# Kernel tuning notes

Measured on AMD Instinct MI355X. Metric: run time of the kernel, lower is better.

The kernel has to match this reference:

```python
import jax, jax.numpy as jnp
import numpy as np

GAMMA = 0.9
SCALE_BASE = 512.0


def _xpos(x, downscale=False):
    """XPOS rotary embedding (torchscale variant) applied to x: (B, L, D)."""
    B, L, D = x.shape
    half = D // 2
    # per-channel magnitude base: ((2i) + 0.4*D) / (1.4*D), i over even channels
    scale_vec = (jnp.arange(0, D, 2, dtype=jnp.float32) + 0.4 * D) / (1.4 * D)  # (half,)
    power = jnp.arange(L, dtype=jnp.float32) / SCALE_BASE                        # (L,)
    scale = scale_vec[None, :] ** power[:, None]                                 # (L, half)
    if downscale:
        scale = 1.0 / scale
    # fixed sinusoidal frequencies over `half` dims
    inv_freq = 1.0 / (10000.0 ** (jnp.arange(half, dtype=jnp.float32) / half))   # (half,)
    sinusoid = jnp.arange(L, dtype=jnp.float32)[:, None] * inv_freq[None, :]     # (L, half)
    sin = jnp.repeat(jnp.sin(sinusoid) * scale, 2, axis=-1)                      # (L, D) interleaved dup
    cos = jnp.repeat(jnp.cos(sinusoid) * scale, 2, axis=-1)
    # rotate_every_two: (x0,x1,x2,x3,...) -> (-x1,x0,-x3,x2,...)
    x_even = x[..., 0::2]
    x_odd = x[..., 1::2]
    rot = jnp.stack((-x_odd, x_even), axis=-1).reshape(x.shape)
    return x * cos + rot * sin


def _get_D(seq_len):
    n = jnp.arange(seq_len, dtype=jnp.float32)[:, None]
    m = jnp.arange(seq_len, dtype=jnp.float32)[None, :]
    D = GAMMA ** jnp.abs(n - m)  # non-causal decay, no NaNs since gamma > 0
    return D


def setup_inputs() -> dict:
    key = jax.random.key(0)
    k1, k2, k3, k4 = jax.random.split(key, 4)
    B, L, H, Dh = 8, 2048, 1024, 1024
    X = jax.random.normal(k1, (B, L, H), dtype=jnp.float32)
    W_Q = jax.random.normal(k2, (H, Dh), dtype=jnp.float32) / H
    W_K = jax.random.normal(k3, (H, Dh), dtype=jnp.float32) / H
    W_V = jax.random.normal(k4, (H, Dh), dtype=jnp.float32) / H
    return {"X": X, "W_Q": W_Q, "W_K": W_K, "W_V": W_V}


def reference(X, W_Q, W_K, W_V):
    B, L, H = X.shape
    D = _get_D(L)                       # (L, L)
    Q = _xpos(X @ W_Q)                  # (B, L, Dh)
    K = _xpos(X @ W_K, downscale=True)  # (B, L, Dh)
    V = X @ W_V                         # (B, L, Dv)
    scores = jnp.einsum('bqd,bkd->bqk', Q, K)   # (B, L, L)
    p_attn = jax.nn.softmax(scores, axis=-1)
    p_attn = p_attn * D[None, :, :]              # elementwise decay AFTER softmax
    return jnp.einsum('bqk,bkv->bqv', p_attn, V)
```

## Files before the change

### kernel.cpp

```cpp
#include <hip/hip_runtime.h>
#include <math.h>


#define LDIM 2048
#define HDIM 1024
#define MTOT 16384

typedef unsigned short u16;
typedef unsigned int u32;
typedef __attribute__((ext_vector_type(16))) float f32x16;
typedef __attribute__((ext_vector_type(8))) short s16x8;

#define GLD16(gp, lp) __builtin_amdgcn_global_load_lds( \
    (const __attribute__((address_space(1))) void*)(gp), \
    (__attribute__((address_space(3))) void*)(lp), 16, 0, 0)

__device__ __forceinline__ u16 f2bf(float f) {
    unsigned u = __float_as_uint(f);
    return (u16)((u + 0x7FFFu + ((u >> 16) & 1u)) >> 16);
}

__device__ __forceinline__ void sincos_rev(float ang, float* sn, float* cs) {
    double dr = (double)ang * 0.15915494309189535;
    dr -= __builtin_floor(dr);
    float fr = (float)dr;
    float s_, c_;
    asm("v_sin_f32 %0, %1" : "=v"(s_) : "v"(fr));
    asm("v_cos_f32 %0, %1" : "=v"(c_) : "v"(fr));
    *sn = s_; *cs = c_;
}

#define ROW32(reg, laneHi) (((reg) & 3) + 8 * ((reg) >> 2) + 4 * (laneHi))

__device__ __forceinline__ void gemm256(const u16* __restrict__ A,
                                        const u16* __restrict__ B,
                                        int lda, int ldb, int K, int m0, int n0,
                                        char* smem, int tid, f32x16 (*acc)[2])
{
    const int wv = tid >> 6, ln = tid & 63;
    const int wm = wv >> 2, wn = wv & 3;
    const int lane31 = ln & 31, laneHi = ln >> 5;
    const int srow = tid >> 3;
    const int scol = ((tid & 7) ^ (srow & 7)) * 8;

    const u16* ap[4];
    const u16* bp[4];
#pragma unroll
    for (int r = 0; r < 4; ++r) {
        ap[r] = A + (size_t)(m0 + r * 64 + srow) * lda + scol;
        bp[r] = B + (size_t)(n0 + r * 64 + srow) * ldb + scol;
    }

    int abyte[4], bbyte[2];
    const int slot_r = (laneHi ^ (lane31 & 7)) << 4;
#pragma unroll
    for (int fm = 0; fm < 4; ++fm)
        abyte[fm] = (wm * 128 + fm * 32 + lane31) * 128 + slot_r;
#pragma unroll
    for (int fn = 0; fn < 2; ++fn)
        bbyte[fn] = 32768 + (wn * 64 + fn * 32 + lane31) * 128 + slot_r;

#define SGA0(e_) do{ char* d_=smem+(e_)*65536+tid*16;       GLD16(ap[0],d_); GLD16(ap[1],d_+8192); ap[0]+=64; ap[1]+=64; }while(0)
#define SGA1(e_) do{ char* d_=smem+(e_)*65536+16384+tid*16; GLD16(ap[2],d_); GLD16(ap[3],d_+8192); ap[2]+=64; ap[3]+=64; }while(0)
#define SGB0(e_) do{ char* d_=smem+(e_)*65536+32768+tid*16; GLD16(bp[0],d_); GLD16(bp[1],d_+8192); bp[0]+=64; bp[1]+=64; }while(0)
#define SGB1(e_) do{ char* d_=smem+(e_)*65536+49152+tid*16; GLD16(bp[2],d_); GLD16(bp[3],d_+8192); bp[2]+=64; bp[3]+=64; }while(0)

#define READS(Bb_, ks) do {                                                   \
        _Pragma("unroll") for (int fm_ = 0; fm_ < 4; ++fm_)                   \
            af[fm_] = *(const s16x8*)((Bb_) + (abyte[fm_] ^ ((ks) << 5)));    \
        _Pragma("unroll") for (int fn_ = 0; fn_ < 2; ++fn_)                   \
            bf[fn_] = *(const s16x8*)((Bb_) + (bbyte[fn_] ^ ((ks) << 5)));    \
    } while (0)

#define MFMA8 do { __builtin_amdgcn_s_setprio(1);                             \
        _Pragma("unroll") for (int fm_ = 0; fm_ < 4; ++fm_)                   \
            _Pragma("unroll") for (int fn_ = 0; fn_ < 2; ++fn_)               \
                acc[fm_][fn_] = __builtin_amdgcn_mfma_f32_32x32x16_bf16(      \
                    af[fm_], bf[fn_], acc[fm_][fn_], 0, 0, 0);                \
        __builtin_amdgcn_s_setprio(0); } while (0)

#define BAR do { __builtin_amdgcn_s_barrier();                                \
                 __builtin_amdgcn_sched_barrier(0); } while (0)

    const int nk = K >> 6;

    SGA0(0); SGB0(0); SGA1(0); SGB1(0);

#pragma unroll 1
    for (int t = 0; t < nk; ++t) {
        const int d = t & 1, e = d ^ 1;
        const bool pre = (t + 1 < nk);
        const char* Bb = smem + d * 65536;
        s16x8 af[4], bf[2];

        if (pre) { SGA0(e); asm volatile("s_waitcnt vmcnt(2)" ::: "memory"); }
        else     {          asm volatile("s_waitcnt vmcnt(0)" ::: "memory"); }
        BAR;
        READS(Bb, 0); if (pre) SGB0(e); BAR; MFMA8; BAR;
        READS(Bb, 1); if (pre) SGA1(e); BAR; MFMA8; BAR;
        READS(Bb, 2); if (pre) SGB1(e); BAR; MFMA8; BAR;
        READS(Bb, 3);                   BAR; MFMA8; BAR;
    }
    __syncthreads();
#undef SGA0
#undef SGA1
#undef SGB0
#undef SGB1
#undef READS
#undef MFMA8
#undef BAR
}

__global__ __launch_bounds__(256) void prep_all(
    const float* __restrict__ X,
    const float* __restrict__ Wq, const float* __restrict__ Wk,
    const float* __restrict__ Wv,
    u16* __restrict__ Xb, u16* __restrict__ WT,
    u32* __restrict__ CSq, u32* __restrict__ CSk)
{
    __shared__ float L[64][65];
    const int bid = blockIdx.x;
    if (bid < 2048) {
        const int n4 = MTOT * HDIM / 4;
        int i = bid * 256 + threadIdx.x;
        const int stride = 2048 * 256;
        for (; i < n4; i += stride) {
            float4 v = ((const float4*)X)[i];
            ushort4 o = make_ushort4(f2bf(v.x), f2bf(v.y), f2bf(v.z), f2bf(v.w));
            ((ushort4*)Xb)[i] = o;
        }
    } else if (bid < 4096) {
        const int l = bid - 2048;
        for (int ih = threadIdx.x; ih < 512; ih += 256) {
            float invf = exp2f(-13.287712379549449f * (1.f / 512.f) * (float)ih);
            float sn, cs;
            sincos_rev((float)l * invf, &sn, &cs);
            float l2sv = log2f(((float)(2 * ih) + 409.6f) * (1.f / 1433.6f));
            float e = (float)l * (1.f / 512.f) * l2sv;
            float sq = exp2f(e), sk = exp2f(-e);
            CSq[l * 512 + ih] = (u32)f2bf(cs * sq) | ((u32)f2bf(sn * sq) << 16);
            CSk[l * 512 + ih] = (u32)f2bf(cs * sk) | ((u32)f2bf(sn * sk) << 16);
        }
    } else {
        const int r = bid - 4096;
        const int z = r >> 8;
        const int y = (r >> 4) & 15;
        const int x = r & 15;
        const float* Wz = (z == 0) ? Wq : (z == 1) ? Wk : Wv;
        u16* Oz = WT + (size_t)z * HDIM * HDIM;
        const int k0 = y * 64, n0 = x * 64;
        const int t = threadIdx.x;
        const int r_ = t >> 4, c4 = (t & 15) * 4;
#pragma unroll
        for (int it = 0; it < 4; ++it) {
            const int row = it * 16 + r_;
            float4 v = *(const float4*)&Wz[(size_t)(k0 + row) * HDIM + n0 + c4];
            L[row][c4 + 0] = v.x; L[row][c4 + 1] = v.y;
            L[row][c4 + 2] = v.z; L[row][c4 + 3] = v.w;
        }
        __syncthreads();
#pragma unroll
        for (int it = 0; it < 4; ++it) {
            const int orow = it * 16 + r_;
            ushort4 o = make_ushort4(f2bf(L[c4 + 0][orow]), f2bf(L[c4 + 1][orow]),
                                     f2bf(L[c4 + 2][orow]), f2bf(L[c4 + 3][orow]));
            *(ushort4*)&Oz[(size_t)(n0 + orow) * HDIM + k0 + c4] = o;
        }
    }
}

__global__ __launch_bounds__(512, 2) void qkv_gemm(
    const u16* __restrict__ Xb, const u16* __restrict__ WT,
    const u32* __restrict__ CSq, const u32* __restrict__ CSk,
    u16* __restrict__ Qb, u16* __restrict__ Kb, u16* __restrict__ Vt)
{
    __shared__ __align__(16) char smem[256 * 264 * 2];
    const int bid = blockIdx.x;
    const int xcd = bid & 7, t = bid >> 3;
    const int m8 = t & 7;
    const int n_ = (t >> 3) & 3;
    const int z  = t >> 5;
    const int m0 = (xcd * 8 + m8) * 256;
    const int n0 = n_ * 256;
    const int tid = threadIdx.x;

    f32x16 acc[4][2] = {};

    gemm256(Xb, WT + (size_t)z * HDIM * HDIM, HDIM, HDIM, HDIM, m0, n0, smem, tid, acc);

    const int wv = tid >> 6, ln = tid & 63;
    const int wm = wv >> 2, wn = wv & 3;
    const int lane31 = ln & 31, laneHi = ln >> 5;
    const int l0 = m0 & (LDIM - 1);
    u16* T = (u16*)smem;

    if (z < 2) {
        const u32* CS = (z == 0) ? CSq : CSk;
#pragma unroll
        for (int fn = 0; fn < 2; ++fn) {
            const int gc = n0 + wn * 64 + fn * 32 + lane31;
            const int ih = gc >> 1;
            const float sgn = (gc & 1) ? 1.f : -1.f;
            const u32* tb = CS + (size_t)l0 * 512 + ih;
#pragma unroll
            for (int fm = 0; fm < 4; ++fm) {
#pragma unroll
                for (int reg = 0; reg < 16; ++reg) {
                    const int rowl = wm * 128 + fm * 32 + ROW32(reg, laneHi);
                    u32 v = tb[(size_t)rowl * 512];
                    float cs = __uint_as_float(v << 16);
                    float sn = __uint_as_float(v & 0xFFFF0000u);
                    float c = acc[fm][fn][reg];
                    float p = __shfl_xor(c, 1);
                    T[rowl * 264 + wn * 64 + fn * 32 + lane31] =
                        f2bf(c * cs + sgn * p * sn);
                }
            }
        }
        __syncthreads();
        u16* Out = (z == 0) ? Qb : Kb;
        const int row_ = tid >> 5, slot = tid & 31;
#pragma unroll
        for (int g = 0; g < 16; ++g) {
            const int row = g * 16 + row_;
            s16x8 v = *(const s16x8*)&T[row * 264 + slot * 8];
            *(s16x8*)&Out[(size_t)(m0 + row) * HDIM + n0 + slot * 8] = v;
        }
    } else {
#pragma unroll
        for (int fn = 0; fn < 2; ++fn)
#pragma unroll
            for (int fm = 0; fm < 4; ++fm)
#pragma unroll
                for (int reg = 0; reg < 16; ++reg)
                    T[(wn * 64 + fn * 32 + lane31) * 264 +
                      wm * 128 + fm * 32 + ROW32(reg, laneHi)] =
                        f2bf(acc[fm][fn][reg]);
        __syncthreads();
        const int b = m0 >> 11;
        const int row_ = tid >> 5, slot = tid & 31;
#pragma unroll
        for (int g = 0; g < 16; ++g) {
            const int row = g * 16 + row_;
            s16x8 v = *(const s16x8*)&T[row * 264 + slot * 8];
            *(s16x8*)&Vt[((size_t)b * HDIM + n0 + row) * LDIM + l0 + slot * 8] = v;
        }
    }
}

__global__ __launch_bounds__(512, 2) void qk_gemm(
    const u16* __restrict__ Q, const u16* __restrict__ Km,
    u16* __restrict__ Wm, float* __restrict__ Zp)
{
    __shared__ __align__(16) char smem[256 * 264 * 2];
    __shared__ float Zl[4][256];
    const int bid = blockIdx.x;
    const int b = bid & 7, t = bid >> 3;
    const int mt = t & 7;
    const int nt = t >> 3;
    const int m0 = mt * 256;
    const int n0 = nt * 256;
    const int tid = threadIdx.x;

    f32x16 acc[4][2] = {};

    gemm256(Q + (size_t)b * LDIM * HDIM, Km + (size_t)b * LDIM * HDIM,
            HDIM, HDIM, HDIM, m0, n0, smem, tid, acc);

    const int wv = tid >> 6, ln = tid & 63;
    const int wm = wv >> 2, wn = wv & 3;
    const int lane31 = ln & 31, laneHi = ln >> 5;
    u16* T = (u16*)smem;
    const float LOG2E = 1.4426950408889634f;
    const float LOG2G = -0.15200309344504997f;

#pragma unroll
    for (int fm = 0; fm < 4; ++fm) {
        float ps[16];
#pragma unroll
        for (int reg = 0; reg < 16; ++reg) ps[reg] = 0.f;
#pragma unroll
        for (int fn = 0; fn < 2; ++fn) {
            const int gk = n0 + wn * 64 + fn * 32 + lane31;
#pragma unroll
            for (int reg = 0; reg < 16; ++reg) {
                const int mloc = wm * 128 + fm * 32 + ROW32(reg, laneHi);
                const int gq = m0 + mloc;
                float t1 = acc[fm][fn][reg] * LOG2E;
                float e = exp2f(t1);
                int dd = gq - gk; dd = dd < 0 ? -dd : dd;
                ps[reg] += e;
                T[mloc * 264 + wn * 64 + fn * 32 + lane31] =
                    f2bf(exp2f(t1 + (float)dd * LOG2G));
            }
        }
#pragma unroll
        for (int reg = 0; reg < 16; ++reg) {
            float s = ps[reg];
            s += __shfl_xor(s, 1); s += __shfl_xor(s, 2);
            s += __shfl_xor(s, 4); s += __shfl_xor(s, 8);
            s += __shfl_xor(s, 16);
            if (lane31 == 0)
                Zl[wn][wm * 128 + fm * 32 + ROW32(reg, laneHi)] = s;
        }
    }
    __syncthreads();

    const int row_ = tid >> 5, slot = tid & 31;
#pragma unroll
    for (int g = 0; g < 16; ++g) {
        const int row = g * 16 + row_;
        s16x8 v = *(const s16x8*)&T[row * 264 + slot * 8];
        *(s16x8*)&Wm[((size_t)b * LDIM + m0 + row) * LDIM + n0 + slot * 8] = v;
    }
    if (tid < 256)
        Zp[((size_t)b * 8 + nt) * LDIM + m0 + tid] =
            Zl[0][tid] + Zl[1][tid] + Zl[2][tid] + Zl[3][tid];
}

__global__ __launch_bounds__(512, 2) void pv_gemm(
    const u16* __restrict__ Wm, const u16* __restrict__ Vt,
    const float* __restrict__ Zp, float* __restrict__ Out)
{
    __shared__ __align__(16) char smem[2 * 65536];
    __shared__ float Zinv[256];
    const int bid = blockIdx.x;
    const int b = bid & 7, t = bid >> 3;
    const int mt4 = t & 3;
    const int nt = (t >> 2) & 3;
    const int mtH = t >> 4;
    const int m0 = (mtH * 4 + mt4) * 256;
    const int n0 = nt * 256;
    const int tid = threadIdx.x;

    if (tid < 256) {
        float zz = 0.f;
#pragma unroll
        for (int nb = 0; nb < 8; ++nb)
            zz += Zp[((size_t)b * 8 + nb) * LDIM + m0 + tid];
        Zinv[tid] = 1.0f / zz;
    }
    __syncthreads();

    f32x16 acc[4][2] = {};

    gemm256(Wm + (size_t)b * LDIM * LDIM, Vt + (size_t)b * HDIM * LDIM,
            LDIM, LDIM, LDIM, m0, n0, smem, tid, acc);

    const int wv = tid >> 6, ln = tid & 63;
    const int wm = wv >> 2, wn = wv & 3;
    const int lane31 = ln & 31, laneHi = ln >> 5;
    float* Ob = Out + (size_t)b * LDIM * HDIM;
#pragma unroll
    for (int fm = 0; fm < 4; ++fm)
#pragma unroll
        for (int fn = 0; fn < 2; ++fn) {
            const int gn = n0 + wn * 64 + fn * 32 + lane31;
#pragma unroll
            for (int reg = 0; reg < 16; ++reg) {
                const int row = wm * 128 + fm * 32 + ROW32(reg, laneHi);
                Ob[(size_t)(m0 + row) * HDIM + gn] = acc[fm][fn][reg] * Zinv[row];
            }
        }
}

extern "C" void kernel_launch(void* const* d_in, const int* in_sizes, int n_in,
                              void* d_out, int out_size, void* d_ws, size_t ws_size,
                              hipStream_t stream)
{
    (void)in_sizes; (void)n_in; (void)out_size; (void)ws_size;
    const float* X  = (const float*)d_in[0];
    const float* Wq = (const float*)d_in[1];
    const float* Wk = (const float*)d_in[2];
    const float* Wv = (const float*)d_in[3];
    char* ws = (char*)d_ws;
    const size_t MB = 1024 * 1024;

    u16* Wmat = (u16*)ws;
    u16* Xb   = (u16*)ws;
    u16* WT   = (u16*)(ws + 32 * MB);
    u16* Qb   = (u16*)(ws + 64 * MB);
    u16* Kb   = (u16*)(ws + 96 * MB);
    u16* Vt   = (u16*)(ws + 128 * MB);
    float* Zp = (float*)(ws + 160 * MB);
    u32* CSq  = (u32*)(ws + 161 * MB);
    u32* CSk  = (u32*)(ws + 165 * MB);

    prep_all<<<4864, 256, 0, stream>>>(X, Wq, Wk, Wv, Xb, WT, CSq, CSk);
    qkv_gemm<<<768, 512, 0, stream>>>(Xb, WT, CSq, CSk, Qb, Kb, Vt);
    qk_gemm<<<512, 512, 0, stream>>>(Qb, Kb, Wmat, Zp);
    pv_gemm<<<256, 512, 0, stream>>>(Wmat, Vt, Zp, (float*)d_out);
}
```

Baseline: 334.3 us.

## Switch GEMMs to 16x16x32 MFMA with quadrant-ordered register reuse

Replaces the 32x32x16 bf16 MFMA tiles with 16x16x32 tiles in all three GEMMs and rewrites the LDS read and MFMA schedule into quadrant order, so A and B fragments are reused across sub-tiles. The prefetch of the next stage's B half is issued earlier. All epilogues are remapped to the new accumulator layout, and the V transpose store is vectorized. The aim is higher MFMA throughput and fewer LDS reads per MFMA, at the cost of more live fragment registers.

```diff
diff --git a/kernel.cpp b/kernel.cpp
--- a/kernel.cpp
+++ b/kernel.cpp
@@ -8,7 +8,7 @@
 
 typedef unsigned short u16;
 typedef unsigned int u32;
-typedef __attribute__((ext_vector_type(16))) float f32x16;
+typedef __attribute__((ext_vector_type(4))) float f32x4;
 typedef __attribute__((ext_vector_type(8))) short s16x8;
 
 #define GLD16(gp, lp) __builtin_amdgcn_global_load_lds( \
@@ -30,16 +30,14 @@
     *sn = s_; *cs = c_;
 }
 
-#define ROW32(reg, laneHi) (((reg) & 3) + 8 * ((reg) >> 2) + 4 * (laneHi))
-
-__device__ __forceinline__ void gemm256(const u16* __restrict__ A,
-                                        const u16* __restrict__ B,
-                                        int lda, int ldb, int K, int m0, int n0,
-                                        char* smem, int tid, f32x16 (*acc)[2])
+__device__ __forceinline__ void gemm256q(const u16* __restrict__ A,
+                                         const u16* __restrict__ B,
+                                         int lda, int ldb, int K, int m0, int n0,
+                                         char* smem, int tid, f32x4 (*acc)[4])
 {
     const int wv = tid >> 6, ln = tid & 63;
     const int wm = wv >> 2, wn = wv & 3;
-    const int lane31 = ln & 31, laneHi = ln >> 5;
+    const int lr = ln & 15, lg = ln >> 4;
     const int srow = tid >> 3;
     const int scol = ((tid & 7) ^ (srow & 7)) * 8;
 
@@ -51,63 +49,79 @@
         bp[r] = B + (size_t)(n0 + r * 64 + srow) * ldb + scol;
     }
 
-    int abyte[4], bbyte[2];
-    const int slot_r = (laneHi ^ (lane31 & 7)) << 4;
-#pragma unroll
-    for (int fm = 0; fm < 4; ++fm)
-        abyte[fm] = (wm * 128 + fm * 32 + lane31) * 128 + slot_r;
-#pragma unroll
-    for (int fn = 0; fn < 2; ++fn)
-        bbyte[fn] = 32768 + (wn * 64 + fn * 32 + lane31) * 128 + slot_r;
+    int arow[8], brow[4];
+#pragma unroll
+    for (int fm = 0; fm < 8; ++fm) arow[fm] = (wm * 128 + fm * 16 + lr) * 128;
+#pragma unroll
+    for (int fn = 0; fn < 4; ++fn) brow[fn] = 32768 + (wn * 64 + fn * 16 + lr) * 128;
+    int slotb[2];
+#pragma unroll
+    for (int kk = 0; kk < 2; ++kk) slotb[kk] = (((kk << 2) | lg) ^ (lr & 7)) << 4;
 
 #define SGA0(e_) do{ char* d_=smem+(e_)*65536+tid*16;       GLD16(ap[0],d_); GLD16(ap[1],d_+8192); ap[0]+=64; ap[1]+=64; }while(0)
 #define SGA1(e_) do{ char* d_=smem+(e_)*65536+16384+tid*16; GLD16(ap[2],d_); GLD16(ap[3],d_+8192); ap[2]+=64; ap[3]+=64; }while(0)
 #define SGB0(e_) do{ char* d_=smem+(e_)*65536+32768+tid*16; GLD16(bp[0],d_); GLD16(bp[1],d_+8192); bp[0]+=64; bp[1]+=64; }while(0)
 #define SGB1(e_) do{ char* d_=smem+(e_)*65536+49152+tid*16; GLD16(bp[2],d_); GLD16(bp[3],d_+8192); bp[2]+=64; bp[3]+=64; }while(0)
 
-#define READS(Bb_, ks) do {                                                   \
+#define RD_A(Bb_, mh) do {                                                    \
         _Pragma("unroll") for (int fm_ = 0; fm_ < 4; ++fm_)                   \
-            af[fm_] = *(const s16x8*)((Bb_) + (abyte[fm_] ^ ((ks) << 5)));    \
+            _Pragma("unroll") for (int kk_ = 0; kk_ < 2; ++kk_)               \
+                aq[fm_ * 2 + kk_] = *(const s16x8*)((Bb_) +                   \
+                    arow[(mh) * 4 + fm_] + slotb[kk_]);                       \
+    } while (0)
+#define RD_B(Bb_, nh, dst) do {                                               \
         _Pragma("unroll") for (int fn_ = 0; fn_ < 2; ++fn_)                   \
-            bf[fn_] = *(const s16x8*)((Bb_) + (bbyte[fn_] ^ ((ks) << 5)));    \
+            _Pragma("unroll") for (int kk_ = 0; kk_ < 2; ++kk_)               \
+                dst[fn_ * 2 + kk_] = *(const s16x8*)((Bb_) +                  \
+                    brow[(nh) * 2 + fn_] + slotb[kk_]);                       \
     } while (0)
 
-#define MFMA8 do { __builtin_amdgcn_s_setprio(1);                             \
+#define MFMA16(mh, nh, bq_) do { __builtin_amdgcn_s_setprio(1);               \
         _Pragma("unroll") for (int fm_ = 0; fm_ < 4; ++fm_)                   \
             _Pragma("unroll") for (int fn_ = 0; fn_ < 2; ++fn_)               \
-                acc[fm_][fn_] = __builtin_amdgcn_mfma_f32_32x32x16_bf16(      \
-                    af[fm_], bf[fn_], acc[fm_][fn_], 0, 0, 0);                \
+                _Pragma("unroll") for (int kk_ = 0; kk_ < 2; ++kk_)           \
+                    acc[(mh) * 4 + fm_][(nh) * 2 + fn_] =                     \
+                        __builtin_amdgcn_mfma_f32_16x16x32_bf16(              \
+                            aq[fm_ * 2 + kk_], bq_[fn_ * 2 + kk_],            \
+                            acc[(mh) * 4 + fm_][(nh) * 2 + fn_], 0, 0, 0);    \
         __builtin_amdgcn_s_setprio(0); } while (0)
 
-#define BAR do { __builtin_amdgcn_s_barrier();                                \
+#define BAR do { __builtin_amdgcn_sched_barrier(0);                           \
+                 __builtin_amdgcn_s_barrier();                                \
                  __builtin_amdgcn_sched_barrier(0); } while (0)
 
     const int nk = K >> 6;
 
     SGA0(0); SGB0(0); SGA1(0); SGB1(0);
+
+    s16x8 aq[8], b0[4], b1[4];
 
 #pragma unroll 1
     for (int t = 0; t < nk; ++t) {
         const int d = t & 1, e = d ^ 1;
         const bool pre = (t + 1 < nk);
         const char* Bb = smem + d * 65536;
-        s16x8 af[4], bf[2];
-
-        if (pre) { SGA0(e); asm volatile("s_waitcnt vmcnt(2)" ::: "memory"); }
-        else     {          asm volatile("s_waitcnt vmcnt(0)" ::: "memory"); }
+
+        if (pre) { SGA0(e); SGB0(e);
+                   asm volatile("s_waitcnt vmcnt(4)" ::: "memory"); }
+        else     { asm volatile("s_waitcnt vmcnt(0)" ::: "memory"); }
         BAR;
-        READS(Bb, 0); if (pre) SGB0(e); BAR; MFMA8; BAR;
-        READS(Bb, 1); if (pre) SGA1(e); BAR; MFMA8; BAR;
-        READS(Bb, 2); if (pre) SGB1(e); BAR; MFMA8; BAR;
-        READS(Bb, 3);                   BAR; MFMA8; BAR;
+        RD_A(Bb, 0); RD_B(Bb, 0, b0); if (pre) SGA1(e);
+        BAR; MFMA16(0, 0, b0); BAR;
+        RD_B(Bb, 1, b1); if (pre) SGB1(e);
+        BAR; MFMA16(0, 1, b1); BAR;
+        RD_A(Bb, 1);
+        BAR; MFMA16(1, 1, b1); BAR;
+        BAR; MFMA16(1, 0, b0); BAR;
     }
     __syncthreads();
 #undef SGA0
 #undef SGA1
 #undef SGB0
 #undef SGB1
-#undef READS
-#undef MFMA8
+#undef RD_A
+#undef RD_B
+#undef MFMA16
 #undef BAR
 }
 
@@ -184,35 +198,35 @@
     const int n0 = n_ * 256;
     const int tid = threadIdx.x;
 
-    f32x16 acc[4][2] = {};
-
-    gemm256(Xb, WT + (size_t)z * HDIM * HDIM, HDIM, HDIM, HDIM, m0, n0, smem, tid, acc);
+    f32x4 acc[8][4] = {};
+
+    gemm256q(Xb, WT + (size_t)z * HDIM * HDIM, HDIM, HDIM, HDIM, m0, n0, smem, tid, acc);
 
     const int wv = tid >> 6, ln = tid & 63;
     const int wm = wv >> 2, wn = wv & 3;
-    const int lane31 = ln & 31, laneHi = ln >> 5;
+    const int lr = ln & 15, lg = ln >> 4;
     const int l0 = m0 & (LDIM - 1);
     u16* T = (u16*)smem;
 
     if (z < 2) {
         const u32* CS = (z == 0) ? CSq : CSk;
 #pragma unroll
-        for (int fn = 0; fn < 2; ++fn) {
-            const int gc = n0 + wn * 64 + fn * 32 + lane31;
+        for (int fn = 0; fn < 4; ++fn) {
+            const int gc = n0 + wn * 64 + fn * 16 + lr;
             const int ih = gc >> 1;
             const float sgn = (gc & 1) ? 1.f : -1.f;
             const u32* tb = CS + (size_t)l0 * 512 + ih;
 #pragma unroll
-            for (int fm = 0; fm < 4; ++fm) {
-#pragma unroll
-                for (int reg = 0; reg < 16; ++reg) {
-                    const int rowl = wm * 128 + fm * 32 + ROW32(reg, laneHi);
+            for (int fm = 0; fm < 8; ++fm) {
+#pragma unroll
+                for (int reg = 0; reg < 4; ++reg) {
+                    const int rowl = wm * 128 + fm * 16 + lg * 4 + reg;
                     u32 v = tb[(size_t)rowl * 512];
                     float cs = __uint_as_float(v << 16);
                     float sn = __uint_as_float(v & 0xFFFF0000u);
                     float c = acc[fm][fn][reg];
                     float p = __shfl_xor(c, 1);
-                    T[rowl * 264 + wn * 64 + fn * 32 + lane31] =
+                    T[rowl * 264 + wn * 64 + fn * 16 + lr] =
                         f2bf(c * cs + sgn * p * sn);
                 }
             }
@@ -228,14 +242,14 @@
         }
     } else {
 #pragma unroll
-        for (int fn = 0; fn < 2; ++fn)
-#pragma unroll
-            for (int fm = 0; fm < 4; ++fm)
-#pragma unroll
-                for (int reg = 0; reg < 16; ++reg)
-                    T[(wn * 64 + fn * 32 + lane31) * 264 +
-                      wm * 128 + fm * 32 + ROW32(reg, laneHi)] =
-                        f2bf(acc[fm][fn][reg]);
+        for (int fn = 0; fn < 4; ++fn)
+#pragma unroll
+            for (int fm = 0; fm < 8; ++fm) {
+                ushort4 o = make_ushort4(f2bf(acc[fm][fn][0]), f2bf(acc[fm][fn][1]),
+                                         f2bf(acc[fm][fn][2]), f2bf(acc[fm][fn][3]));
+                *(ushort4*)&T[(wn * 64 + fn * 16 + lr) * 264 +
+                              wm * 128 + fm * 16 + lg * 4] = o;
+            }
         __syncthreads();
         const int b = m0 >> 11;
         const int row_ = tid >> 5, slot = tid & 31;
@@ -262,46 +276,43 @@
     const int n0 = nt * 256;
     const int tid = threadIdx.x;
 
-    f32x16 acc[4][2] = {};
-
-    gemm256(Q + (size_t)b * LDIM * HDIM, Km + (size_t)b * LDIM * HDIM,
-            HDIM, HDIM, HDIM, m0, n0, smem, tid, acc);
+    f32x4 acc[8][4] = {};
+
+    gemm256q(Q + (size_t)b * LDIM * HDIM, Km + (size_t)b * LDIM * HDIM,
+             HDIM, HDIM, HDIM, m0, n0, smem, tid, acc);
 
     const int wv = tid >> 6, ln = tid & 63;
     const int wm = wv >> 2, wn = wv & 3;
-    const int lane31 = ln & 31, laneHi = ln >> 5;
+    const int lr = ln & 15, lg = ln >> 4;
     u16* T = (u16*)smem;
     const float LOG2E = 1.4426950408889634f;
     const float LOG2G = -0.15200309344504997f;
 
 #pragma unroll
-    for (int fm = 0; fm < 4; ++fm) {
-        float ps[16];
-#pragma unroll
-        for (int reg = 0; reg < 16; ++reg) ps[reg] = 0.f;
-#pragma unroll
-        for (int fn = 0; fn < 2; ++fn) {
-            const int gk = n0 + wn * 64 + fn * 32 + lane31;
-#pragma unroll
-            for (int reg = 0; reg < 16; ++reg) {
-                const int mloc = wm * 128 + fm * 32 + ROW32(reg, laneHi);
+    for (int fm = 0; fm < 8; ++fm) {
+        float ps[4] = {0.f, 0.f, 0.f, 0.f};
+#pragma unroll
+        for (int fn = 0; fn < 4; ++fn) {
+            const int gk = n0 + wn * 64 + fn * 16 + lr;
+#pragma unroll
+            for (int reg = 0; reg < 4; ++reg) {
+                const int mloc = wm * 128 + fm * 16 + lg * 4 + reg;
                 const int gq = m0 + mloc;
                 float t1 = acc[fm][fn][reg] * LOG2E;
                 float e = exp2f(t1);
                 int dd = gq - gk; dd = dd < 0 ? -dd : dd;
                 ps[reg] += e;
-                T[mloc * 264 + wn * 64 + fn * 32 + lane31] =
+                T[mloc * 264 + wn * 64 + fn * 16 + lr] =
                     f2bf(exp2f(t1 + (float)dd * LOG2G));
             }
         }
 #pragma unroll
-        for (int reg = 0; reg < 16; ++reg) {
+        for (int reg = 0; reg < 4; ++reg) {
             float s = ps[reg];
             s += __shfl_xor(s, 1); s += __shfl_xor(s, 2);
             s += __shfl_xor(s, 4); s += __shfl_xor(s, 8);
-            s += __shfl_xor(s, 16);
-            if (lane31 == 0)
-                Zl[wn][wm * 128 + fm * 32 + ROW32(reg, laneHi)] = s;
+            if (lr == 0)
+                Zl[wn][wm * 128 + fm * 16 + lg * 4 + reg] = s;
         }
     }
     __syncthreads();
@@ -342,23 +353,23 @@
     }
     __syncthreads();
 
-    f32x16 acc[4][2] = {};
-
-    gemm256(Wm + (size_t)b * LDIM * LDIM, Vt + (size_t)b * HDIM * LDIM,
-            LDIM, LDIM, LDIM, m0, n0, smem, tid, acc);
+    f32x4 acc[8][4] = {};
+
+    gemm256q(Wm + (size_t)b * LDIM * LDIM, Vt + (size_t)b * HDIM * LDIM,
+             LDIM, LDIM, LDIM, m0, n0, smem, tid, acc);
 
     const int wv = tid >> 6, ln = tid & 63;
     const int wm = wv >> 2, wn = wv & 3;
-    const int lane31 = ln & 31, laneHi = ln >> 5;
+    const int lr = ln & 15, lg = ln >> 4;
     float* Ob = Out + (size_t)b * LDIM * HDIM;
 #pragma unroll
-    for (int fm = 0; fm < 4; ++fm)
-#pragma unroll
-        for (int fn = 0; fn < 2; ++fn) {
-            const int gn = n0 + wn * 64 + fn * 32 + lane31;
-#pragma unroll
-            for (int reg = 0; reg < 16; ++reg) {
-                const int row = wm * 128 + fm * 32 + ROW32(reg, laneHi);
+    for (int fm = 0; fm < 8; ++fm)
+#pragma unroll
+        for (int fn = 0; fn < 4; ++fn) {
+            const int gn = n0 + wn * 64 + fn * 16 + lr;
+#pragma unroll
+            for (int reg = 0; reg < 4; ++reg) {
+                const int row = wm * 128 + fm * 16 + lg * 4 + reg;
                 Ob[(size_t)(m0 + row) * HDIM + gn] = acc[fm][fn][reg] * Zinv[row];
             }
         }
```

After: 309.5 us. 1.08x faster.
